# Kernel optimization log

Hardware: AMD Instinct MI355X
Metric: run time of the kernel (lower is better)

The kernel has to match this reference:

```python
import jax, jax.numpy as jnp
import numpy as np
import math

B, T, C = 2, 2048, 1024
NH = 16
HD = C // NH

def setup_inputs() -> dict:
    key = jax.random.key(0)
    ks = jax.random.split(key, 3)
    scale = 0.02
    return {
        "x": jax.random.normal(ks[0], (B, T, C), dtype=jnp.float32),
        "Wqkv": jax.random.normal(ks[1], (C, 3 * C), dtype=jnp.float32) * scale,
        "bqkv": jnp.zeros((3 * C,), dtype=jnp.float32),
        "Wproj": jax.random.normal(ks[2], (C, C), dtype=jnp.float32) * scale,
        "bproj": jnp.zeros((C,), dtype=jnp.float32),
    }

def reference(x, Wqkv, bqkv, Wproj, bproj):
    b, t, c = x.shape
    qkv = x @ Wqkv + bqkv                      # (B,T,3C)
    qkv = qkv.reshape(b, t, 3, NH, HD)
    q = jnp.transpose(qkv[:, :, 0], (0, 2, 1, 3))  # (B,H,T,D)
    k = jnp.transpose(qkv[:, :, 1], (0, 2, 1, 3))
    v = jnp.transpose(qkv[:, :, 2], (0, 2, 1, 3))
    att = jnp.einsum('bhqd,bhkd->bhqk', q, k) / math.sqrt(HD)
    causal = jnp.tril(jnp.ones((t, t), dtype=bool))
    att = jnp.where(causal[None, None], att, jnp.float32(-jnp.inf))
    att = jax.nn.softmax(att, axis=-1)
    y = jnp.einsum('bhqk,bhkd->bhqd', att, v)  # (B,H,T,D)
    y = jnp.transpose(y, (0, 2, 1, 3)).reshape(b, t, c)
    return y @ Wproj + bproj
```

## Files before the change

kernel.cpp:

```cpp
#include <hip/hip_runtime.h>


typedef __attribute__((ext_vector_type(8))) short short8;
typedef __attribute__((ext_vector_type(4))) short short4v;
typedef __attribute__((ext_vector_type(4))) float f32x4;
typedef __attribute__((ext_vector_type(2))) unsigned int u32x2;

#define MFMA16(a, b, c) __builtin_amdgcn_mfma_f32_16x16x32_bf16((a), (b), (c), 0, 0, 0)
#define MFMA16K16(a, b, c) __builtin_amdgcn_mfma_f32_16x16x16bf16_1k((a), (b), (c), 0, 0, 0)

__device__ __forceinline__ unsigned short f2bf(float f) {
  unsigned u = __builtin_bit_cast(unsigned, f);
  u += 0x7fffu + ((u >> 16) & 1u);
  return (unsigned short)(u >> 16);
}

__device__ __forceinline__ unsigned short f2bf_fast(float f) {
  return (unsigned short)((__builtin_bit_cast(unsigned, f) + 0x8000u) >> 16);
}

#if __has_builtin(__builtin_amdgcn_cvt_pk_bf16_f32)
typedef __attribute__((ext_vector_type(2))) __bf16 bf16x2;
__device__ __forceinline__ short4v pack_bf16x4(float a, float b, float c, float d) {
  bf16x2 lo = __builtin_amdgcn_cvt_pk_bf16_f32(a, b);
  bf16x2 hi = __builtin_amdgcn_cvt_pk_bf16_f32(c, d);
  u32x2 t;
  t[0] = __builtin_bit_cast(unsigned, lo);
  t[1] = __builtin_bit_cast(unsigned, hi);
  return __builtin_bit_cast(short4v, t);
}
#else
__device__ __forceinline__ short4v pack_bf16x4(float a, float b, float c, float d) {
  short4v r;
  r[0] = (short)f2bf_fast(a); r[1] = (short)f2bf_fast(b);
  r[2] = (short)f2bf_fast(c); r[3] = (short)f2bf_fast(d);
  return r;
}
#endif

__device__ __forceinline__ short4v pack_rne4(float a, float b, float c, float d) {
  short4v r;
  r[0] = (short)f2bf(a); r[1] = (short)f2bf(b);
  r[2] = (short)f2bf(c); r[3] = (short)f2bf(d);
  return r;
}

__device__ __forceinline__ void gl2lds16(const void* g, void* l) {
  __builtin_amdgcn_global_load_lds(
      (__attribute__((address_space(1))) void*)g,
      (__attribute__((address_space(3))) void*)l,
      16, 0, 0);
}

__global__ __launch_bounds__(256)
void prep(const float* __restrict__ x, unsigned short* __restrict__ xb,
          const float* __restrict__ Wqkv, unsigned short* __restrict__ wqkvT,
          const float* __restrict__ Wproj, unsigned short* __restrict__ wprojT) {
  __shared__ float tile[64][65];
  const int bx = blockIdx.x, tid = threadIdx.x;
  if (bx < 4096) {
    const int i = (bx * 256 + tid) * 4;
    float4 f = *(const float4*)(x + i);
    unsigned long long r = (unsigned long long)f2bf(f.x)
        | ((unsigned long long)f2bf(f.y) << 16)
        | ((unsigned long long)f2bf(f.z) << 32)
        | ((unsigned long long)f2bf(f.w) << 48);
    *(unsigned long long*)(xb + i) = r;
    return;
  }
  const float* W;
  unsigned short* WT;
  int n0, k0, N;
  if (bx < 4864) {
    const int idx = bx - 4096;
    W = Wqkv; WT = wqkvT; N = 3072;
    n0 = (idx % 48) * 64; k0 = (idx / 48) * 64;
  } else {
    const int idx = bx - 4864;
    W = Wproj; WT = wprojT; N = 1024;
    n0 = (idx % 16) * 64; k0 = (idx / 16) * 64;
  }
  const int K = 1024;
  const int c = tid & 63, rbase = tid >> 6;
#pragma unroll
  for (int i = 0; i < 16; ++i) {
    int r = i * 4 + rbase;
    tile[r][c] = W[(size_t)(k0 + r) * N + n0 + c];
  }
  __syncthreads();
#pragma unroll
  for (int i = 0; i < 16; ++i) {
    int r = i * 4 + rbase;
    WT[(size_t)(n0 + r) * K + k0 + c] = f2bf(tile[c][r]);
  }
}

template <int MT>
__device__ __forceinline__ void gemm_core(
    const unsigned short* __restrict__ gA,
    const unsigned short* __restrict__ gB,
    unsigned short* As, unsigned short* Bs,
    int Kdim, int wave, int quad, int lr, int wm, int wn,
    f32x4 (&acc)[MT / 32][4]) {
  constexpr int IF = MT / 32;
  constexpr int RA = MT / 32;
  const size_t rstep = (size_t)32 * Kdim;
  for (int k0 = 0; k0 < Kdim; k0 += 64) {
#pragma unroll
    for (int rd = 0; rd < RA; ++rd)
      gl2lds16(gA + k0 + rd * rstep, As + rd * 2048 + wave * 512);
#pragma unroll
    for (int rd = 0; rd < 4; ++rd)
      gl2lds16(gB + k0 + rd * rstep, Bs + rd * 2048 + wave * 512);
    __syncthreads();
#pragma unroll
    for (int s = 0; s < 2; ++s) {
      const int sw = ((s * 4 + quad) ^ (lr & 7)) * 8;
      short8 a[IF], b[4];
#pragma unroll
      for (int i = 0; i < IF; ++i)
        a[i] = *(const short8*)(As + (wm * (MT / 2) + i * 16 + lr) * 64 + sw);
#pragma unroll
      for (int j = 0; j < 4; ++j)
        b[j] = *(const short8*)(Bs + (wn * 64 + j * 16 + lr) * 64 + sw);
#pragma unroll
      for (int i = 0; i < IF; ++i)
#pragma unroll
        for (int j = 0; j < 4; ++j)
          acc[i][j] = MFMA16(a[i], b[j], acc[i][j]);
    }
    __syncthreads();
  }
}

template <int EPI, int MT>
__global__ __launch_bounds__(256)
void gemm_bt(const unsigned short* __restrict__ A,
             const unsigned short* __restrict__ BT,
             const float* __restrict__ bias,
             float* __restrict__ outF,
             unsigned short* __restrict__ q_out,
             unsigned short* __restrict__ k_out,
             unsigned short* __restrict__ vT_out,
             int Ndim, int Kdim) {
  constexpr int IF = MT / 32;
  __shared__ __align__(16) unsigned short As[MT * 64];
  __shared__ __align__(16) unsigned short Bs[128 * 64];
  const int tid = threadIdx.x;
  const int wave = tid >> 6, lane = tid & 63;
  const int quad = lane >> 4, lr = lane & 15;
  const int wm = wave >> 1, wn = wave & 1;
  const int m0 = blockIdx.y * MT, n0 = blockIdx.x * 128;

  const int r_l = tid >> 3;
  const int cg = (tid & 7) ^ (r_l & 7);
  const unsigned short* gA = A + (size_t)(m0 + r_l) * Kdim + cg * 8;
  const unsigned short* gB = BT + (size_t)(n0 + r_l) * Kdim + cg * 8;

  f32x4 acc[IF][4] = {};
  gemm_core<MT>(gA, gB, As, Bs, Kdim, wave, quad, lr, wm, wn, acc);

  const int row_t = wm * (MT / 2) + quad * 4;
  const int col_t = wn * 64 + lr;
  if constexpr (EPI == 0) {
    const int sec = n0 >> 10;
    const float scl = (sec == 0) ? 0.18033688f : 1.0f;
#pragma unroll
    for (int j = 0; j < 4; ++j) {
      const int n = n0 + col_t + j * 16;
      const float bi = bias[n];
      const int nn = n & 1023, h = nn >> 6, d = nn & 63;
#pragma unroll
      for (int i = 0; i < IF; ++i) {
        const int m_base = m0 + row_t + i * 16;
        const int bb = m_base >> 11, t0 = m_base & 2047;
        const int bh = bb * 16 + h;
        if (sec == 2) {
          short4v pk = pack_rne4(acc[i][j][0] + bi, acc[i][j][1] + bi,
                                 acc[i][j][2] + bi, acc[i][j][3] + bi);
          *(short4v*)(vT_out + ((size_t)bh * 64 + d) * 2048 + t0) = pk;
        } else {
          unsigned short* dst = (sec == 0 ? q_out : k_out) + (size_t)bh * 131072 + t0 * 64 + d;
#pragma unroll
          for (int r = 0; r < 4; ++r)
            dst[r * 64] = f2bf((acc[i][j][r] + bi) * scl);
        }
      }
    }
  } else {
#pragma unroll
    for (int i = 0; i < IF; ++i)
#pragma unroll
      for (int r = 0; r < 4; ++r) {
        const int m = m0 + row_t + i * 16 + r;
#pragma unroll
        for (int j = 0; j < 4; ++j) {
          const int n = n0 + col_t + j * 16;
          outF[(size_t)m * Ndim + n] = acc[i][j][r] + bias[n];
        }
      }
  }
}

__global__ __launch_bounds__(256, 4)
void attn(const unsigned short* __restrict__ qbuf,
          const unsigned short* __restrict__ kbuf,
          const unsigned short* __restrict__ vT,
          unsigned short* __restrict__ yb) {
  __shared__ __align__(16) unsigned short Ks[2][4096];
  __shared__ __align__(16) unsigned short Vs[2][4096];
  const int tid = threadIdx.x, wave = tid >> 6, lane = tid & 63;
  const int quad = lane >> 4, lr = lane & 15;
  const int bh = blockIdx.x;
  const int by = blockIdx.y;
  int qt;
  if (by < 8)       qt = 31 - by;
  else if (by < 16) qt = by - 8;
  else if (by < 24) qt = 39 - by;
  else              qt = by - 16;
  const int qrow0 = qt * 64;

  const unsigned short* qp0 = qbuf + (size_t)bh * 131072;
  const unsigned short* kp0 = kbuf + (size_t)bh * 131072;
  const unsigned short* vp0 = vT   + (size_t)bh * 131072;

  short8 aq[2];
  {
    const unsigned short* qp =
        qp0 + (size_t)(qrow0 + wave * 16 + lr) * 64 + quad * 8;
    aq[0] = *(const short8*)qp;
    aq[1] = *(const short8*)(qp + 32);
  }

  short4v ones4;
#pragma unroll
  for (int i = 0; i < 4; ++i) ones4[i] = (short)0x3F80;

  const int sr = tid >> 3;
  const int scg = (tid & 7) ^ (sr & 7);
  int kbase[2];
#pragma unroll
  for (int h = 0; h < 2; ++h)
    kbase[h] = lr * 64 + (((quad + 4 * h) ^ (lr & 7)) << 3);
  int vbase[4];
#pragma unroll
  for (int kb = 0; kb < 4; ++kb)
    vbase[kb] = lr * 64 + (((2 * kb + (quad >> 1)) ^ (lr & 7)) << 3) + (quad & 1) * 4;

  f32x4 o[4] = {};
  f32x4 lacc = {};

  auto stage = [&](int buf, int kt) {
    const unsigned short* kg = kp0 + (size_t)(kt * 64 + sr) * 64 + scg * 8;
    const unsigned short* vg = vp0 + (size_t)sr * 2048 + kt * 64 + scg * 8;
    gl2lds16(kg,             &Ks[buf][wave * 512]);
    gl2lds16(kg + 32 * 64,   &Ks[buf][2048 + wave * 512]);
    gl2lds16(vg,             &Vs[buf][wave * 512]);
    gl2lds16(vg + 32 * 2048, &Vs[buf][2048 + wave * 512]);
  };

  const int dlast = qt;
  stage(0, 0);
  int cur = 0;
  for (int kt = 0; kt <= dlast; ++kt) {
    __builtin_amdgcn_s_waitcnt(0x0F70);
    __builtin_amdgcn_s_barrier();
    if (kt + 1 <= dlast) stage(cur ^ 1, kt + 1);
    const unsigned short* Kb = Ks[cur];
    const unsigned short* Vb = Vs[cur];
    short8 bk[4][2];
#pragma unroll
    for (int jt = 0; jt < 4; ++jt) {
      bk[jt][0] = *(const short8*)(Kb + jt * 1024 + kbase[0]);
      bk[jt][1] = *(const short8*)(Kb + jt * 1024 + kbase[1]);
    }
    f32x4 s[4] = {};
    __builtin_amdgcn_s_setprio(1);
#pragma unroll
    for (int jt = 0; jt < 4; ++jt) {
      s[jt] = MFMA16(bk[jt][0], aq[0], s[jt]);
      s[jt] = MFMA16(bk[jt][1], aq[1], s[jt]);
    }
    __builtin_amdgcn_s_setprio(0);
    short4v pa[4];
    if (kt == dlast) {
      const int qloc = wave * 16 + lr;
#pragma unroll
      for (int jt = 0; jt < 4; ++jt) {
        float p[4];
#pragma unroll
        for (int r = 0; r < 4; ++r) {
          p[r] = __builtin_amdgcn_exp2f(s[jt][r]);
          if (jt * 16 + quad * 4 + r > qloc) p[r] = 0.f;
        }
        pa[jt] = pack_bf16x4(p[0], p[1], p[2], p[3]);
      }
    } else {
#pragma unroll
      for (int jt = 0; jt < 4; ++jt) {
        float p[4];
#pragma unroll
        for (int r = 0; r < 4; ++r) p[r] = __builtin_amdgcn_exp2f(s[jt][r]);
        pa[jt] = pack_bf16x4(p[0], p[1], p[2], p[3]);
      }
    }
    __builtin_amdgcn_s_setprio(1);
#pragma unroll
    for (int kb = 0; kb < 4; ++kb)
      lacc = MFMA16K16(ones4, pa[kb], lacc);
#pragma unroll
    for (int kb = 0; kb < 4; ++kb)
#pragma unroll
      for (int jd = 0; jd < 4; ++jd) {
        const short4v bv = *(const short4v*)(Vb + jd * 1024 + vbase[kb]);
        o[jd] = MFMA16K16(pa[kb], bv, o[jd]);
      }
    __builtin_amdgcn_s_setprio(0);
    cur ^= 1;
  }

  const int b = bh >> 4, h = bh & 15;
  float inv[4];
#pragma unroll
  for (int r = 0; r < 4; ++r)
    inv[r] = __builtin_amdgcn_rcpf(__shfl(lacc[0], quad * 4 + r));
#pragma unroll
  for (int jd = 0; jd < 4; ++jd)
#pragma unroll
    for (int r = 0; r < 4; ++r) {
      const int t = qrow0 + wave * 16 + quad * 4 + r;
      yb[((size_t)b * 2048 + t) * 1024 + h * 64 + jd * 16 + lr] =
          f2bf(o[jd][r] * inv[r]);
    }
}

extern "C" void kernel_launch(void* const* d_in, const int* in_sizes, int n_in,
                              void* d_out, int out_size, void* d_ws, size_t ws_size,
                              hipStream_t stream) {
  const float* x     = (const float*)d_in[0];
  const float* Wqkv  = (const float*)d_in[1];
  const float* bqkv  = (const float*)d_in[2];
  const float* Wproj = (const float*)d_in[3];
  const float* bproj = (const float*)d_in[4];
  float* out = (float*)d_out;

  char* ws = (char*)d_ws;
  unsigned short* xb     = (unsigned short*)(ws);
  unsigned short* wqkvT  = (unsigned short*)(ws + 8388608);
  unsigned short* wprojT = (unsigned short*)(ws + 14680064);
  unsigned short* qbuf   = (unsigned short*)(ws + 16777216);
  unsigned short* kbuf   = (unsigned short*)(ws + 25165824);
  unsigned short* vTbuf  = (unsigned short*)(ws + 33554432);
  unsigned short* ybuf   = (unsigned short*)(ws + 41943040);

  prep<<<5120, 256, 0, stream>>>(x, xb, Wqkv, wqkvT, Wproj, wprojT);
  gemm_bt<0, 128><<<dim3(24, 32), 256, 0, stream>>>(xb, wqkvT, bqkv, nullptr,
                                                    qbuf, kbuf, vTbuf, 3072, 1024);
  attn<<<dim3(32, 32), 256, 0, stream>>>(qbuf, kbuf, vTbuf, ybuf);
  gemm_bt<1, 64><<<dim3(8, 64), 256, 0, stream>>>(ybuf, wprojT, bproj, out,
                                                  nullptr, nullptr, nullptr, 1024, 1024);
}
```

Before: 182.2 us.

## Split long causal attention query tiles into two KV chunks with combine kernel

Query tiles 16-31 now have their key range split across two blocks, which write unnormalized partial outputs and row sums to workspace. A new combine kernel adds the two partials, normalizes them and writes bf16. This shortens the longest per-block critical path and evens out causal work imbalance. The cost is an extra kernel launch and fp32 partial traffic. Because softmax here uses no running max, the partials can simply be summed.

```diff
diff --git a/kernel.cpp b/kernel.cpp
--- a/kernel.cpp
+++ b/kernel.cpp
@@ -206,18 +206,19 @@
 void attn(const unsigned short* __restrict__ qbuf,
           const unsigned short* __restrict__ kbuf,
           const unsigned short* __restrict__ vT,
-          unsigned short* __restrict__ yb) {
+          unsigned short* __restrict__ yb,
+          float* __restrict__ o_part,
+          float* __restrict__ l_part) {
   __shared__ __align__(16) unsigned short Ks[2][4096];
   __shared__ __align__(16) unsigned short Vs[2][4096];
   const int tid = threadIdx.x, wave = tid >> 6, lane = tid & 63;
   const int quad = lane >> 4, lr = lane & 15;
   const int bh = blockIdx.x;
-  const int by = blockIdx.y;
-  int qt;
-  if (by < 8)       qt = 31 - by;
-  else if (by < 16) qt = by - 8;
-  else if (by < 24) qt = 39 - by;
-  else              qt = by - 16;
+  const int jj = 47 - (int)blockIdx.y;
+  int qt, kstart, kend, chunk;
+  if (jj >= 32)      { qt = jj - 16; chunk = 1; kstart = (qt + 1) >> 1; kend = qt + 1; }
+  else if (jj >= 16) { qt = jj;      chunk = 0; kstart = 0; kend = (qt + 1) >> 1; }
+  else               { qt = jj;      chunk = -1; kstart = 0; kend = qt + 1; }
   const int qrow0 = qt * 64;
 
   const unsigned short* qp0 = qbuf + (size_t)bh * 131072;
@@ -259,13 +260,12 @@
     gl2lds16(vg + 32 * 2048, &Vs[buf][2048 + wave * 512]);
   };
 
-  const int dlast = qt;
-  stage(0, 0);
+  stage(0, kstart);
   int cur = 0;
-  for (int kt = 0; kt <= dlast; ++kt) {
+  for (int kt = kstart; kt < kend; ++kt) {
     __builtin_amdgcn_s_waitcnt(0x0F70);
     __builtin_amdgcn_s_barrier();
-    if (kt + 1 <= dlast) stage(cur ^ 1, kt + 1);
+    if (kt + 1 < kend) stage(cur ^ 1, kt + 1);
     const unsigned short* Kb = Ks[cur];
     const unsigned short* Vb = Vs[cur];
     short8 bk[4][2];
@@ -283,7 +283,7 @@
     }
     __builtin_amdgcn_s_setprio(0);
     short4v pa[4];
-    if (kt == dlast) {
+    if (kt == qt) {
       const int qloc = wave * 16 + lr;
 #pragma unroll
       for (int jt = 0; jt < 4; ++jt) {
@@ -319,19 +319,54 @@
     cur ^= 1;
   }
 
+  if (chunk < 0) {
+    const int b = bh >> 4, h = bh & 15;
+    float inv[4];
+#pragma unroll
+    for (int r = 0; r < 4; ++r)
+      inv[r] = __builtin_amdgcn_rcpf(__shfl(lacc[0], quad * 4 + r));
+#pragma unroll
+    for (int jd = 0; jd < 4; ++jd)
+#pragma unroll
+      for (int r = 0; r < 4; ++r) {
+        const int t = qrow0 + wave * 16 + quad * 4 + r;
+        yb[((size_t)b * 2048 + t) * 1024 + h * 64 + jd * 16 + lr] =
+            f2bf(o[jd][r] * inv[r]);
+      }
+  } else {
+    const int slot = (bh * 16 + (qt - 16)) * 2 + chunk;
+    float* op = o_part + ((size_t)slot * 64 + wave * 16) * 64;
+#pragma unroll
+    for (int jd = 0; jd < 4; ++jd)
+#pragma unroll
+      for (int r = 0; r < 4; ++r)
+        op[(quad * 4 + r) * 64 + jd * 16 + lr] = o[jd][r];
+    if (lane < 16) l_part[slot * 64 + wave * 16 + lane] = lacc[0];
+  }
+}
+
+__global__ __launch_bounds__(256)
+void combine(const float* __restrict__ o_part, const float* __restrict__ l_part,
+             unsigned short* __restrict__ yb) {
+  const int bh = blockIdx.x, qtl = blockIdx.y;
+  const int tid = threadIdx.x;
+  const int row = tid >> 2, dd = (tid & 3) * 16;
+  const int qt = 16 + qtl;
+  const int slotA = (bh * 16 + qtl) * 2, slotB = slotA + 1;
+  const float l = l_part[slotA * 64 + row] + l_part[slotB * 64 + row];
+  const float inv = __builtin_amdgcn_rcpf(l);
+  const float* oa = o_part + ((size_t)slotA * 64 + row) * 64 + dd;
+  const float* ob = o_part + ((size_t)slotB * 64 + row) * 64 + dd;
   const int b = bh >> 4, h = bh & 15;
-  float inv[4];
-#pragma unroll
-  for (int r = 0; r < 4; ++r)
-    inv[r] = __builtin_amdgcn_rcpf(__shfl(lacc[0], quad * 4 + r));
-#pragma unroll
-  for (int jd = 0; jd < 4; ++jd)
-#pragma unroll
-    for (int r = 0; r < 4; ++r) {
-      const int t = qrow0 + wave * 16 + quad * 4 + r;
-      yb[((size_t)b * 2048 + t) * 1024 + h * 64 + jd * 16 + lr] =
-          f2bf(o[jd][r] * inv[r]);
-    }
+  unsigned short* yp = yb + ((size_t)b * 2048 + qt * 64 + row) * 1024 + h * 64 + dd;
+#pragma unroll
+  for (int j = 0; j < 16; j += 4) {
+    const float4 a4 = *(const float4*)(oa + j);
+    const float4 b4 = *(const float4*)(ob + j);
+    short4v pk = pack_rne4((a4.x + b4.x) * inv, (a4.y + b4.y) * inv,
+                           (a4.z + b4.z) * inv, (a4.w + b4.w) * inv);
+    *(short4v*)(yp + j) = pk;
+  }
 }
 
 extern "C" void kernel_launch(void* const* d_in, const int* in_sizes, int n_in,
@@ -352,11 +387,14 @@
   unsigned short* kbuf   = (unsigned short*)(ws + 25165824);
   unsigned short* vTbuf  = (unsigned short*)(ws + 33554432);
   unsigned short* ybuf   = (unsigned short*)(ws + 41943040);
+  float* o_part          = (float*)(ws + 50331648);
+  float* l_part          = (float*)(ws + 67108864);
 
   prep<<<5120, 256, 0, stream>>>(x, xb, Wqkv, wqkvT, Wproj, wprojT);
   gemm_bt<0, 128><<<dim3(24, 32), 256, 0, stream>>>(xb, wqkvT, bqkv, nullptr,
                                                     qbuf, kbuf, vTbuf, 3072, 1024);
-  attn<<<dim3(32, 32), 256, 0, stream>>>(qbuf, kbuf, vTbuf, ybuf);
+  attn<<<dim3(32, 48), 256, 0, stream>>>(qbuf, kbuf, vTbuf, ybuf, o_part, l_part);
+  combine<<<dim3(32, 16), 256, 0, stream>>>(o_part, l_part, ybuf);
   gemm_bt<1, 64><<<dim3(8, 64), 256, 0, stream>>>(ybuf, wprojT, bproj, out,
                                                   nullptr, nullptr, nullptr, 1024, 1024);
 }
```

Result: faster. 176.9 us (median of 3 runs) (-2.9%).
